# Performance work log

Measured on AMD Instinct MI355X. Metric: run time of the kernel, lower is better.

Reference implementation:

```python
import jax, jax.numpy as jnp
import numpy as np

Q_DIM = 1024
KV_DIM = 1024
D_ATTN = 1024
N_HEADS = 16
HDIM = D_ATTN // N_HEADS
LOOKBACK = 3
KW = LOOKBACK + 1
SCALE = HDIM ** -0.5

B, LQ, LKV = 4, 4096, 512


def setup_inputs() -> dict:
    key = jax.random.key(0)
    ks = jax.random.split(key, 6)
    q = jax.random.normal(ks[0], (B, LQ, Q_DIM), dtype=jnp.float32)
    kv_src = jax.random.normal(ks[1], (B, LKV, KV_DIM), dtype=jnp.float32)
    seg_id = jnp.sort(jax.random.randint(ks[2], (B, LQ), 0, LKV), axis=-1)
    # Linear weights (torch convention: y = x @ W.T), no bias
    Wq = jax.random.normal(ks[3], (D_ATTN, Q_DIM), dtype=jnp.float32) * (Q_DIM ** -0.5)
    Wkv = jax.random.normal(ks[4], (2 * D_ATTN, KV_DIM), dtype=jnp.float32) * (KV_DIM ** -0.5)
    Wo = jax.random.normal(ks[5], (Q_DIM, D_ATTN), dtype=jnp.float32) * (D_ATTN ** -0.5)
    return {"q": q, "kv_src": kv_src, "seg_id": seg_id, "Wq": Wq, "Wkv": Wkv, "Wo": Wo}


def _split_heads(x):
    # (B, L, D) -> (B, H, L, Dh)
    b, l, _ = x.shape
    return x.reshape(b, l, N_HEADS, HDIM).transpose(0, 2, 1, 3)


def reference(q, kv_src, seg_id, Wq, Wkv, Wo):
    b, lq, _ = q.shape
    lkv = kv_src.shape[1]

    qh = _split_heads(q @ Wq.T)                      # (B,H,Lq,Dh)
    kv = kv_src @ Wkv.T                              # (B,Lkv,2*D)
    k, v = jnp.split(kv, 2, axis=-1)
    kh = _split_heads(k)                             # (B,H,Lkv,Dh)
    vh = _split_heads(v)

    offsets = jnp.arange(KW)                         # (Kw,)
    gather = seg_id[:, :, None] - offsets            # (B,Lq,Kw)
    neg_mask = gather < 0
    gc = jnp.clip(gather, 0, lkv - 1)                # (B,Lq,Kw)

    b_idx = jnp.arange(b)[:, None, None]
    # advanced indexing: (B,Lq,Kw,H,Dh) -> transpose to (B,H,Lq,Kw,Dh)
    k_sel = kh[b_idx, :, gc].transpose(0, 3, 1, 2, 4)
    v_sel = vh[b_idx, :, gc].transpose(0, 3, 1, 2, 4)

    scores = jnp.einsum('bhqd,bhqkd->bhqk', qh, k_sel) * SCALE
    neg_inf = jnp.finfo(scores.dtype).min
    scores = jnp.where(neg_mask[:, None, :, :], neg_inf, scores)
    probs = jax.nn.softmax(scores, axis=-1)
    out = jnp.einsum('bhqk,bhqkd->bhqd', probs, v_sel)   # (B,H,Lq,Dh)
    out = out.transpose(0, 2, 1, 3).reshape(b, lq, D_ATTN)
    return out @ Wo.T                                # (B,Lq,q_dim)
```

## Files before the change

### kernel.cpp

```cpp
#include <hip/hip_runtime.h>
#include <math.h>

#define NH 16
#define HDIM 64
#define D_ATTN 1024
#define KW 4
#define ATT_SCALE 0.125f
#define LKV_C 512
#define LQ_C 4096
#define B_C 4

typedef _Float16 f16;
typedef _Float16 f16x8 __attribute__((ext_vector_type(8)));
typedef _Float16 f16x4 __attribute__((ext_vector_type(4)));
typedef float f32x4 __attribute__((ext_vector_type(4)));

typedef __attribute__((address_space(3))) unsigned int as3_uint;
typedef __attribute__((address_space(1))) const unsigned int as1_uint;

__device__ __forceinline__ void gld_lds16(const f16* g, f16* l) {
    __builtin_amdgcn_global_load_lds((as1_uint*)g, (as3_uint*)l, 16, 0, 0);
}

__global__ __launch_bounds__(256) void split_hi(const float* __restrict__ x,
                                                f16* __restrict__ hi, int n4) {
    int i = blockIdx.x * 256 + threadIdx.x;
    if (i >= n4) return;
    float4 v = ((const float4*)x)[i];
    ((f16x4*)hi)[i] = (f16x4){(f16)v.x, (f16)v.y, (f16)v.z, (f16)v.w};
}

__global__ __launch_bounds__(256) void gemm_f16(const f16* __restrict__ A,
                                                const f16* __restrict__ B,
                                                float* __restrict__ C,
                                                int M, int N, int K) {
    __shared__ f16 smem[2 * 128 * 32];
    f16* sA = smem;
    f16* sB = smem + 4096;

    const int t = threadIdx.x;
    const int w = t >> 6;
    const int lane = t & 63;
    const int bm = blockIdx.y * 128;
    const int bn = blockIdx.x * 128;
    const int wm = (w & 1) * 64;
    const int wn = (w >> 1) * 64;

    f32x4 acc[4][4] = {};

    const int frow = lane & 15;
    const int fchunk = lane >> 4;

    const int srow = t >> 2;
    const int chunk = (t & 3) ^ ((t >> 3) & 3);
    const size_t aoff0 = (size_t)(bm + srow) * K + chunk * 8;
    const size_t aoff1 = (size_t)(bm + 64 + srow) * K + chunk * 8;
    const size_t boff0 = (size_t)(bn + srow) * K + chunk * 8;
    const size_t boff1 = (size_t)(bn + 64 + srow) * K + chunk * 8;
    const unsigned loff0 = (w * 64) * 8;
    const unsigned loff1 = (256 + w * 64) * 8;

    gld_lds16(A + aoff0, sA + loff0);  gld_lds16(A + aoff1, sA + loff1);
    gld_lds16(B + boff0, sB + loff0);  gld_lds16(B + boff1, sB + loff1);

    for (int k0 = 0; k0 < K; k0 += 32) {
        __syncthreads();

        f16x8 a[4], b[4];
        #pragma unroll
        for (int i = 0; i < 4; ++i) {
            const int r = wm + i * 16 + frow;
            a[i] = *(const f16x8*)(sA + r * 32 + (fchunk ^ ((r >> 1) & 3)) * 8);
        }
        #pragma unroll
        for (int j = 0; j < 4; ++j) {
            const int r = wn + j * 16 + frow;
            b[j] = *(const f16x8*)(sB + r * 32 + (fchunk ^ ((r >> 1) & 3)) * 8);
        }

        __syncthreads();

        if (k0 + 32 < K) {
            const int kn = k0 + 32;
            gld_lds16(A + aoff0 + kn, sA + loff0);  gld_lds16(A + aoff1 + kn, sA + loff1);
            gld_lds16(B + boff0 + kn, sB + loff0);  gld_lds16(B + boff1 + kn, sB + loff1);
        }

        #pragma unroll
        for (int i = 0; i < 4; ++i)
            #pragma unroll
            for (int j = 0; j < 4; ++j)
                acc[i][j] = __builtin_amdgcn_mfma_f32_16x16x32_f16(a[i], b[j], acc[i][j], 0, 0, 0);
    }

    const int rbase = bm + wm + (lane >> 4) * 4;
    const int cbase = bn + wn + (lane & 15);
    #pragma unroll
    for (int i = 0; i < 4; ++i)
        #pragma unroll
        for (int j = 0; j < 4; ++j)
            #pragma unroll
            for (int r = 0; r < 4; ++r)
                C[(size_t)(rbase + i * 16 + r) * N + cbase + j * 16] = acc[i][j][r];
}

__global__ __launch_bounds__(256) void attn_kernel(const float* __restrict__ qh,
                                                   const float* __restrict__ kvp,
                                                   const int* __restrict__ seg_id,
                                                   f16* __restrict__ attn_o) {
    const int wid = blockIdx.x * 4 + (threadIdx.x >> 6);
    const int lane = threadIdx.x & 63;
    const int row = wid >> 2;
    const int hg  = wid & 3;
    const int hh = lane >> 4;
    const int s  = lane & 15;
    const int head = hg * 4 + hh;
    const int b = row >> 12;
    const int seg = seg_id[row];
    const int dbase = head * HDIM + 4 * s;

    const float4 q4 = *(const float4*)(qh + (size_t)row * D_ATTN + dbase);
    const float* kvb = kvp + (size_t)b * LKV_C * (2 * D_ATTN);

    float sc[KW];
    #pragma unroll
    for (int w = 0; w < KW; ++w) {
        const int j = seg - w;
        float p = 0.f;
        if (j >= 0) {
            const float4 k4 = *(const float4*)(kvb + (size_t)j * (2 * D_ATTN) + dbase);
            p = q4.x * k4.x + q4.y * k4.y + q4.z * k4.z + q4.w * k4.w;
        }
        p += __shfl_xor(p, 1);
        p += __shfl_xor(p, 2);
        p += __shfl_xor(p, 4);
        p += __shfl_xor(p, 8);
        sc[w] = (j >= 0) ? p * ATT_SCALE : -1e30f;
    }

    const float m = fmaxf(fmaxf(sc[0], sc[1]), fmaxf(sc[2], sc[3]));
    float e[KW], sum = 0.f;
    #pragma unroll
    for (int w = 0; w < KW; ++w) {
        e[w] = __expf(sc[w] - m);
        sum += e[w];
    }
    const float inv = 1.f / sum;

    float4 o = make_float4(0.f, 0.f, 0.f, 0.f);
    #pragma unroll
    for (int w = 0; w < KW; ++w) {
        const int j = seg - w;
        if (j >= 0) {
            const float4 v4 = *(const float4*)(kvb + (size_t)j * (2 * D_ATTN) + D_ATTN + dbase);
            const float c = e[w] * inv;
            o.x = fmaf(c, v4.x, o.x);
            o.y = fmaf(c, v4.y, o.y);
            o.z = fmaf(c, v4.z, o.z);
            o.w = fmaf(c, v4.w, o.w);
        }
    }

    *(f16x4*)(attn_o + (size_t)row * D_ATTN + dbase) =
        (f16x4){(f16)o.x, (f16)o.y, (f16)o.z, (f16)o.w};
}

extern "C" void kernel_launch(void* const* d_in, const int* in_sizes, int n_in,
                              void* d_out, int out_size, void* d_ws, size_t ws_size,
                              hipStream_t stream) {
    const float* q      = (const float*)d_in[0];
    const float* kv_src = (const float*)d_in[1];
    const int*   seg    = (const int*)  d_in[2];
    const float* Wq     = (const float*)d_in[3];
    const float* Wkv    = (const float*)d_in[4];
    const float* Wo     = (const float*)d_in[5];
    float* out = (float*)d_out;

    const int M  = B_C * LQ_C;
    const int Mk = B_C * LKV_C;

    f16* q_hi   = (f16*)d_ws;
    f16* kvs_hi = q_hi   + (size_t)M * D_ATTN;
    f16* Wq_hi  = kvs_hi + (size_t)Mk * 1024;
    f16* Wkv_hi = Wq_hi  + 1024 * 1024;
    f16* Wo_hi  = Wkv_hi + 2048 * 1024;
    float* kvp  = (float*)(Wo_hi + 1024 * 1024);
    f16* attn_o = q_hi;
    float* qh = (float*)d_out;

    split_hi<<<(M * D_ATTN) / 1024, 256, 0, stream>>>(q, q_hi, (M * D_ATTN) / 4);
    split_hi<<<(Mk * 1024) / 1024, 256, 0, stream>>>(kv_src, kvs_hi, (Mk * 1024) / 4);
    split_hi<<<(1024 * 1024) / 1024, 256, 0, stream>>>(Wq, Wq_hi, (1024 * 1024) / 4);
    split_hi<<<(2048 * 1024) / 1024, 256, 0, stream>>>(Wkv, Wkv_hi, (2048 * 1024) / 4);
    split_hi<<<(1024 * 1024) / 1024, 256, 0, stream>>>(Wo, Wo_hi, (1024 * 1024) / 4);

    gemm_f16<<<dim3(1024 / 128, M / 128), 256, 0, stream>>>(q_hi, Wq_hi, qh, M, 1024, 1024);
    gemm_f16<<<dim3(2048 / 128, Mk / 128), 256, 0, stream>>>(kvs_hi, Wkv_hi, kvp, Mk, 2048, 1024);
    attn_kernel<<<(M * NH) / 16, 256, 0, stream>>>(qh, kvp, seg, attn_o);
    gemm_f16<<<dim3(1024 / 128, M / 128), 256, 0, stream>>>(attn_o, Wo_hi, out, M, 1024, 1024);
}
```

Measured before the change: 306.5 us.

## Add 256x256-tile pipelined f16 GEMM for Q and output projections

Adds a new GEMM kernel with 256x256 block tiles, 512 threads, and K=128 double-buffered LDS staging. Loads are interleaved with MFMA quadrants, ordered by explicit vmcnt waits and barriers, with setprio raised around the MFMAs. Blocks are remapped in a grouped order across the grid. The Q and output projection GEMMs use it to gain operand reuse and to overlap global loads with compute, at the cost of 128KB of LDS per block and more register pressure.

```diff
diff --git a/kernel.cpp b/kernel.cpp
--- a/kernel.cpp
+++ b/kernel.cpp
@@ -102,6 +102,128 @@
             #pragma unroll
             for (int r = 0; r < 4; ++r)
                 C[(size_t)(rbase + i * 16 + r) * N + cbase + j * 16] = acc[i][j][r];
+}
+
+__device__ __forceinline__ void stage_half(const f16* __restrict__ g, size_t row0,
+                                           int K, int kcol, f16* l) {
+    const int t = threadIdx.x;
+    #pragma unroll
+    for (int i = 0; i < 2; ++i) {
+        const int idx = i * 512 + t;
+        const int r = idx >> 3;
+        const int qg = (idx & 7) ^ (r & 7);
+        gld_lds16(g + (row0 + r) * (size_t)K + kcol + qg * 8, l + idx * 8);
+    }
+}
+
+#define BAR __builtin_amdgcn_s_barrier()
+#define VM6 asm volatile("s_waitcnt vmcnt(6)" ::: "memory")
+#define VM8 asm volatile("s_waitcnt vmcnt(8)" ::: "memory")
+#define VM0 asm volatile("s_waitcnt vmcnt(0)" ::: "memory")
+
+#define RD_A(S, mh)                                                         \
+    { _Pragma("unroll") for (int mi = 0; mi < 4; ++mi) {                    \
+        const f16* p = (S) + ((mh) * 128 + mi * 32 + arow) * 64;            \
+        a[0][mi] = *(const f16x8*)(p + q0);                                 \
+        a[1][mi] = *(const f16x8*)(p + q1); } }
+
+#define RD_B(S, nh)                                                         \
+    { _Pragma("unroll") for (int ni = 0; ni < 2; ++ni) {                    \
+        const f16* p = (S) + (((nh) * 2 + ni) * 64 + brow) * 64;            \
+        b[0][(nh) * 2 + ni] = *(const f16x8*)(p + q0);                      \
+        b[1][(nh) * 2 + ni] = *(const f16x8*)(p + q1); } }
+
+#define QUAD(mh, nh)                                                        \
+    { __builtin_amdgcn_s_setprio(1);                                        \
+      _Pragma("unroll") for (int mi = 0; mi < 4; ++mi)                      \
+      _Pragma("unroll") for (int ni = 0; ni < 2; ++ni) {                    \
+          f32x4& c = acc[(mh) * 4 + mi][(nh) * 2 + ni];                     \
+          c = __builtin_amdgcn_mfma_f32_16x16x32_f16(a[0][mi], b[0][(nh) * 2 + ni], c, 0, 0, 0); \
+          c = __builtin_amdgcn_mfma_f32_16x16x32_f16(a[1][mi], b[1][(nh) * 2 + ni], c, 0, 0, 0); \
+      }                                                                     \
+      __builtin_amdgcn_s_setprio(0); }
+
+__global__ __launch_bounds__(512, 2) void gemm256(const f16* __restrict__ A,
+                                                  const f16* __restrict__ B,
+                                                  float* __restrict__ C,
+                                                  int M, int N, int K) {
+    __shared__ __align__(16) f16 smem[4 * 16384];
+    f16* const sA0 = smem;
+    f16* const sA1 = smem + 16384;
+    f16* const sB0 = smem + 32768;
+    f16* const sB1 = smem + 49152;
+
+    const int t = threadIdx.x;
+    const int lane = t & 63;
+    const int w = t >> 6;
+    const int wr = w >> 2;
+    const int wc = w & 3;
+    const int frow = lane & 15;
+    const int fc = lane >> 4;
+
+    const int nbx = N >> 8;
+    const int nwg = gridDim.x;
+    const int wg = (blockIdx.x & 7) * (nwg >> 3) + (blockIdx.x >> 3);
+    const int bm = (wg / nbx) << 8;
+    const int bn = (wg % nbx) << 8;
+
+    const int arow = wr * 16 + frow;
+    const int brow = wc * 16 + frow;
+    const int q0 = (fc ^ (frow & 7)) * 8;
+    const int q1 = ((4 + fc) ^ (frow & 7)) * 8;
+
+    f32x4 acc[8][4] = {};
+    f16x8 a[2][4], b[2][4];
+
+    stage_half(A, bm,       K, 0,  sA0);
+    stage_half(B, bn,       K, 0,  sB0);
+    stage_half(B, bn + 128, K, 0,  sB0 + 8192);
+    stage_half(A, bm + 128, K, 0,  sA0 + 8192);
+    stage_half(A, bm,       K, 64, sA1);
+    stage_half(B, bn,       K, 64, sB1);
+    stage_half(B, bn + 128, K, 64, sB1 + 8192);
+    stage_half(A, bm + 128, K, 64, sA1 + 8192);
+    VM8;
+    BAR;
+
+    const int NT = K >> 7;
+    for (int it = 0; it < NT; ++it) {
+        const bool lastit = (it == NT - 1);
+        const int kc2 = (it * 2 + 2) << 6;
+        const int kc3 = (it * 2 + 3) << 6;
+
+        RD_A(sA0, 0); RD_B(sB0, 0);
+        BAR; QUAD(0, 0); BAR;
+        RD_B(sB0, 1);
+        if (!lastit) { stage_half(A, bm, K, kc2, sA0); stage_half(B, bn, K, kc2, sB0); }
+        BAR; QUAD(0, 1); BAR;
+        RD_A(sA0, 1);
+        if (!lastit) stage_half(B, bn + 128, K, kc2, sB0 + 8192);
+        BAR; QUAD(1, 0); BAR;
+        if (lastit) { VM0; } else { VM6; stage_half(A, bm + 128, K, kc2, sA0 + 8192); }
+        BAR; QUAD(1, 1); BAR;
+
+        RD_A(sA1, 0); RD_B(sB1, 0);
+        BAR; QUAD(0, 0); BAR;
+        RD_B(sB1, 1);
+        if (!lastit) { stage_half(A, bm, K, kc3, sA1); stage_half(B, bn, K, kc3, sB1); }
+        BAR; QUAD(0, 1); BAR;
+        RD_A(sA1, 1);
+        if (!lastit) stage_half(B, bn + 128, K, kc3, sB1 + 8192);
+        BAR; QUAD(1, 0); BAR;
+        if (!lastit) { VM6; stage_half(A, bm + 128, K, kc3, sA1 + 8192); }
+        BAR; QUAD(1, 1); BAR;
+    }
+
+    const size_t rb = (size_t)bm + wr * 16 + ((lane >> 4) << 2);
+    const int cb = bn + wc * 16 + (lane & 15);
+    #pragma unroll
+    for (int m = 0; m < 8; ++m)
+        #pragma unroll
+        for (int n = 0; n < 4; ++n)
+            #pragma unroll
+            for (int rr = 0; rr < 4; ++rr)
+                C[(rb + m * 32 + rr) * N + cb + n * 64] = acc[m][n][rr];
 }
 
 __global__ __launch_bounds__(256) void attn_kernel(const float* __restrict__ qh,
@@ -194,8 +316,8 @@
     split_hi<<<(2048 * 1024) / 1024, 256, 0, stream>>>(Wkv, Wkv_hi, (2048 * 1024) / 4);
     split_hi<<<(1024 * 1024) / 1024, 256, 0, stream>>>(Wo, Wo_hi, (1024 * 1024) / 4);
 
-    gemm_f16<<<dim3(1024 / 128, M / 128), 256, 0, stream>>>(q_hi, Wq_hi, qh, M, 1024, 1024);
+    gemm256<<<(M / 256) * (1024 / 256), 512, 0, stream>>>(q_hi, Wq_hi, qh, M, 1024, 1024);
     gemm_f16<<<dim3(2048 / 128, Mk / 128), 256, 0, stream>>>(kvs_hi, Wkv_hi, kvp, Mk, 2048, 1024);
     attn_kernel<<<(M * NH) / 16, 256, 0, stream>>>(qh, kvp, seg, attn_o);
-    gemm_f16<<<dim3(1024 / 128, M / 128), 256, 0, stream>>>(attn_o, Wo_hi, out, M, 1024, 1024);
-}
+    gemm256<<<(M / 256) * (1024 / 256), 512, 0, stream>>>(attn_o, Wo_hi, out, M, 1024, 1024);
+}
```

Result: faster. 287.6 us (-6.2%).
